# Optimization experiments

Hardware: AMD Instinct MI355X
Metric: run time of the kernel (lower is better)

Reference implementation:

```python
import jax, jax.numpy as jnp
import numpy as np

H = 16          # num_attention_heads
D = 1024        # input_size == hidden_size
HD = D // H     # attention_head_size = 64
EPS = 1e-12


def setup_inputs() -> dict:
    key = jax.random.key(0)
    ks = jax.random.split(key, 12)
    B, S = 4, 2048
    sc = 1.0 / np.sqrt(D)
    return {
        "x": jax.random.normal(ks[0], (B, S, D), jnp.float32),
        "y": jax.random.normal(ks[1], (B, S, D), jnp.float32),
        "Wq": jax.random.normal(ks[2], (D, D), jnp.float32) * sc,
        "bq": jnp.zeros((D,), jnp.float32),
        "Wk": jax.random.normal(ks[3], (D, D), jnp.float32) * sc,
        "bk": jnp.zeros((D,), jnp.float32),
        "Wv": jax.random.normal(ks[4], (D, D), jnp.float32) * sc,
        "bv": jnp.zeros((D,), jnp.float32),
        "Wd": jax.random.normal(ks[5], (D, D), jnp.float32) * sc,
        "bd": jnp.zeros((D,), jnp.float32),
        "gamma": jnp.ones((D,), jnp.float32),
        "beta": jnp.zeros((D,), jnp.float32),
        "debug": 0,
    }


def _split_heads(t):
    B, S, _ = t.shape
    return t.reshape(B, S, H, HD).transpose(0, 2, 1, 3)  # [B,H,S,hd]


def reference(x, y, Wq, bq, Wk, bk, Wv, bv, Wd, bd, gamma, beta, debug):
    # torch Linear: t @ W.T + b
    q = _split_heads(x @ Wq.T + bq)   # query from x
    k = _split_heads(y @ Wk.T + bk)   # key from y
    v = _split_heads(x @ Wv.T + bv)   # value from x (as in source)
    scores = jnp.einsum("bhqd,bhkd->bhqk", q, k) / np.sqrt(HD)
    probs = jax.nn.softmax(scores, axis=-1)  # dropout: eval mode (identity)
    ctx = jnp.einsum("bhqk,bhkd->bhqd", probs, v)
    B, _, S, _ = ctx.shape
    ctx = ctx.transpose(0, 2, 1, 3).reshape(B, S, D)
    h = ctx @ Wd.T + bd               # out_dropout: eval mode (identity)
    h = h + x
    u = h.mean(-1, keepdims=True)
    s = jnp.square(h - u).mean(-1, keepdims=True)
    h = (h - u) / jnp.sqrt(s + EPS)
    return gamma * h + beta
```

## Files before the change

kernel.cpp:

```cpp
#include <hip/hip_runtime.h>
#include <hip/hip_bf16.h>
#include <stdint.h>


typedef unsigned short ushortT;
typedef __attribute__((ext_vector_type(8))) __bf16 bf16x8;
typedef __attribute__((ext_vector_type(4))) float f32x4;
typedef __attribute__((ext_vector_type(16))) float f32x16;
typedef __attribute__((ext_vector_type(8))) unsigned short ushort8;
typedef __attribute__((ext_vector_type(4))) unsigned short ushort4v;

__device__ __forceinline__ unsigned short f2bf(float f) {
  union { float f; unsigned u; } x; x.f = f;
  unsigned r = (x.u + 0x7FFFu + ((x.u >> 16) & 1u)) >> 16;
  return (unsigned short)r;
}

__device__ __forceinline__ unsigned cvtpk_bf16(float lo, float hi) {
  unsigned r;
  asm("v_cvt_pk_bf16_f32 %0, %1, %2" : "=v"(r) : "v"(lo), "v"(hi));
  return r;
}

__device__ __forceinline__ void load_lds16(const void* g, void* l) {
  __builtin_amdgcn_global_load_lds(
      (const __attribute__((address_space(1))) void*)g,
      (__attribute__((address_space(3))) void*)l, 16, 0, 0);
}

__device__ __forceinline__ f32x4 mfma16(bf16x8 a, bf16x8 b, f32x4 c) {
  return __builtin_amdgcn_mfma_f32_16x16x32_bf16(a, b, c, 0, 0, 0);
}
__device__ __forceinline__ f32x16 mfma32(bf16x8 a, bf16x8 b, f32x16 c) {
  return __builtin_amdgcn_mfma_f32_32x32x16_bf16(a, b, c, 0, 0, 0);
}

__global__ __launch_bounds__(256) void k_cvt_all(
    const float* __restrict__ x, const float* __restrict__ y,
    const float* __restrict__ w0, const float* __restrict__ w1,
    const float* __restrict__ w2, const float* __restrict__ w3,
    ushortT* __restrict__ ox, ushortT* __restrict__ oy,
    ushortT* __restrict__ o0, ushortT* __restrict__ o1,
    ushortT* __restrict__ o2, ushortT* __restrict__ o3) {
  int b = blockIdx.x;
  const float* in;
  ushortT* out;
  int blk;
  if (b < 4096) {
    in = x; out = ox; blk = b;
  } else if (b < 8192) {
    in = y; out = oy; blk = b - 4096;
  } else {
    int z = (b - 8192) >> 9;
    blk = (b - 8192) & 511;
    in = (z == 0) ? w0 : (z == 1) ? w1 : (z == 2) ? w2 : w3;
    out = (z == 0) ? o0 : (z == 1) ? o1 : (z == 2) ? o2 : o3;
  }
  int i = blk * 256 + threadIdx.x;
  const float4* p = (const float4*)in;
  float4 u = p[(size_t)i * 2];
  float4 v = p[(size_t)i * 2 + 1];
  ushort8 o;
  o[0] = f2bf(u.x); o[1] = f2bf(u.y); o[2] = f2bf(u.z); o[3] = f2bf(u.w);
  o[4] = f2bf(v.x); o[5] = f2bf(v.y); o[6] = f2bf(v.z); o[7] = f2bf(v.w);
  *(ushort8*)(out + (size_t)i * 8) = o;
}

__global__ __launch_bounds__(256, 2) void k_gemm(
    const ushortT* __restrict__ xbf, const ushortT* __restrict__ ybf,
    const ushortT* __restrict__ wq, const ushortT* __restrict__ wk,
    const ushortT* __restrict__ wv, const ushortT* __restrict__ wd,
    const float* __restrict__ bq, const float* __restrict__ bk,
    const float* __restrict__ bv, const float* __restrict__ bd,
    const ushortT* __restrict__ ctx, const float* __restrict__ xres,
    ushortT* __restrict__ Qo, ushortT* __restrict__ Ko,
    ushortT* __restrict__ Vt, float* __restrict__ Ho, int mode_base) {
  __shared__ ushortT lA[2][128 * 64];
  __shared__ ushortT lB[2][128 * 64];
  const int t = threadIdx.x;
  const int lane = t & 63;
  const int w = t >> 6;
  const int wm = w >> 1, wn = w & 1;
  const int mode = mode_base + blockIdx.z;
  const int flat = blockIdx.x + (blockIdx.y << 3);
  const int xcd = flat & 7, j = flat >> 3;
  const int m0 = (xcd * 8 + (j >> 3)) * 128;
  const int n0 = (j & 7) * 128;

  const ushortT* A = (mode == 1) ? ybf : (mode == 3 ? ctx : xbf);
  const ushortT* W = (mode == 0) ? wq : (mode == 1 ? wk : (mode == 2 ? wv : wd));
  const float* bias = (mode == 0) ? bq : (mode == 1 ? bk : (mode == 2 ? bv : bd));

  f32x4 z = {0.f, 0.f, 0.f, 0.f};
  f32x4 acc[4][4];
#pragma unroll
  for (int i = 0; i < 4; ++i)
#pragma unroll
    for (int j2 = 0; j2 < 4; ++j2) acc[i][j2] = z;

  const int so = t * 16;
  const int srow = so >> 7;
  const int skb = (so & 127) ^ ((srow & 7) << 4);
  const ushortT* asrc = A + (size_t)(m0 + srow) * 1024 + (skb >> 1);
  const ushortT* wsrc = W + (size_t)(n0 + srow) * 1024 + (skb >> 1);

#define GSTAGE(buf, k0)                                                     \
  do {                                                                      \
    _Pragma("unroll")                                                       \
    for (int c = 0; c < 4; ++c) {                                           \
      load_lds16(asrc + (k0) + (size_t)c * 32 * 1024,                       \
                 (char*)&lA[buf][0] + c * 4096 + t * 16);                   \
      load_lds16(wsrc + (k0) + (size_t)c * 32 * 1024,                       \
                 (char*)&lB[buf][0] + c * 4096 + t * 16);                   \
    }                                                                       \
  } while (0)

  GSTAGE(0, 0);
  GSTAGE(1, 64);
  int cur = 0;
  for (int k0 = 0; k0 < 1024; k0 += 64) {
    if (k0 < 960) {
      asm volatile("s_waitcnt vmcnt(8)" ::: "memory");
    } else {
      asm volatile("s_waitcnt vmcnt(0)" ::: "memory");
    }
    __builtin_amdgcn_sched_barrier(0);
    __builtin_amdgcn_s_barrier();
    __builtin_amdgcn_sched_barrier(0);
#pragma unroll
    for (int kk = 0; kk < 2; ++kk) {
      bf16x8 af[4], bfr[4];
#pragma unroll
      for (int i = 0; i < 4; ++i) {
        int arow = wm * 64 + i * 16 + (lane & 15);
        int ak = ((kk * 32 + (lane >> 4) * 8) * 2) ^ ((arow & 7) << 4);
        af[i] = *(const bf16x8*)((const char*)&lA[cur][0] + arow * 128 + ak);
        int brow = wn * 64 + i * 16 + (lane & 15);
        int bk2 = ((kk * 32 + (lane >> 4) * 8) * 2) ^ ((brow & 7) << 4);
        bfr[i] = *(const bf16x8*)((const char*)&lB[cur][0] + brow * 128 + bk2);
      }
      __builtin_amdgcn_s_setprio(1);
#pragma unroll
      for (int i = 0; i < 4; ++i)
#pragma unroll
        for (int j2 = 0; j2 < 4; ++j2)
          acc[i][j2] = mfma16(af[i], bfr[j2], acc[i][j2]);
      __builtin_amdgcn_s_setprio(0);
    }
    __builtin_amdgcn_sched_barrier(0);
    __builtin_amdgcn_s_barrier();
    __builtin_amdgcn_sched_barrier(0);
    if (k0 + 128 < 1024) GSTAGE(cur, k0 + 128);
    cur ^= 1;
  }
#undef GSTAGE

  const int cm = wm * 64 + (lane >> 4) * 4;
  const int cn = wn * 64 + (lane & 15);
  if (mode == 3) {
#pragma unroll
    for (int mi = 0; mi < 4; ++mi)
#pragma unroll
      for (int ni = 0; ni < 4; ++ni) {
        int n = n0 + cn + ni * 16;
        float bn = bias[n];
#pragma unroll
        for (int r = 0; r < 4; ++r) {
          int m = m0 + cm + mi * 16 + r;
          Ho[(size_t)m * 1024 + n] =
              acc[mi][ni][r] + bn + xres[(size_t)m * 1024 + n];
        }
      }
  } else if (mode == 2) {
#pragma unroll
    for (int mi = 0; mi < 4; ++mi)
#pragma unroll
      for (int ni = 0; ni < 4; ++ni) {
        int n = n0 + cn + ni * 16;
        int hh = n >> 6, hd = n & 63;
        float bn = bias[n];
        int m_ = m0 + cm + mi * 16;
        int b = m_ >> 11, s = m_ & 2047;
        ushort4v pk;
#pragma unroll
        for (int r = 0; r < 4; ++r) pk[r] = f2bf(acc[mi][ni][r] + bn);
        *(ushort4v*)&Vt[(((size_t)(b * 16 + hh) * 64 + hd) << 11) + s] = pk;
      }
  } else {
    ushortT* O = (mode == 0) ? Qo : Ko;
    const float qs = (mode == 0) ? 0.18033688011112042f : 1.0f;
#pragma unroll
    for (int mi = 0; mi < 4; ++mi)
#pragma unroll
      for (int ni = 0; ni < 4; ++ni) {
        int n = n0 + cn + ni * 16;
        int hh = n >> 6, hd = n & 63;
        float bn = bias[n];
#pragma unroll
        for (int r = 0; r < 4; ++r) {
          int m = m0 + cm + mi * 16 + r;
          int b = m >> 11, s = m & 2047;
          O[(((size_t)(b * 16 + hh) * 2048 + s) << 6) + hd] =
              f2bf((acc[mi][ni][r] + bn) * qs);
        }
      }
  }
}

__global__ __launch_bounds__(256, 4) void k_attn(const ushortT* __restrict__ Q,
                                                 const ushortT* __restrict__ K,
                                                 const ushortT* __restrict__ Vt,
                                                 ushortT* __restrict__ ctx) {
  __shared__ ushortT lK[2][4096];
  __shared__ ushortT lV[2][4096];
  const int t = threadIdx.x, lane = t & 63, w = t >> 6;
  const int hi = lane >> 5, l31 = lane & 31;
  const int i0 = blockIdx.x;
  const int xcd = i0 & 7, j0 = i0 >> 3;
  const int bh = xcd * 8 + (j0 >> 4);
  const int qt = j0 & 15;
  const int q0 = qt * 128 + w * 32;

  const ushortT* Qb = Q + ((size_t)bh * 2048 + q0) * 64;
  const ushortT* Kb = K + (size_t)bh * 2048 * 64;
  const ushortT* Vb = Vt + (size_t)bh * 64 * 2048;

  bf16x8 qf[4];
#pragma unroll
  for (int dc = 0; dc < 4; ++dc)
    qf[dc] = *(const bf16x8*)(Qb + l31 * 64 + dc * 16 + hi * 8);

  union { unsigned short us[8]; bf16x8 v; } ones_u;
#pragma unroll
  for (int i = 0; i < 8; ++i) ones_u.us[i] = 0x3F80;

  f32x16 accO0, accO1, accL;
#pragma unroll
  for (int i = 0; i < 16; ++i) { accO0[i] = 0.f; accO1[i] = 0.f; accL[i] = 0.f; }

  const int srow = t >> 3;
  const int scolb = ((t & 7) * 16) ^ ((srow & 7) << 4);
  const ushortT* ksrc = Kb + srow * 64 + (scolb >> 1);
  const ushortT* vsrc = Vb + (size_t)srow * 2048 + (scolb >> 1);
  const int swz = (lane & 7) << 4;
  const int hs = (hi * 16) ^ swz;
  const int krowb = l31 * 128;

#define STAGE(buf, kk)                                                        \
  do {                                                                        \
    load_lds16(ksrc + (size_t)(kk) * 64, (char*)&lK[buf][0] + w * 1024);      \
    load_lds16(ksrc + 2048 + (size_t)(kk) * 64,                               \
               (char*)&lK[buf][0] + 4096 + w * 1024);                         \
    load_lds16(vsrc + (kk), (char*)&lV[buf][0] + w * 1024);                   \
    load_lds16(vsrc + 65536 + (kk), (char*)&lV[buf][0] + 4096 + w * 1024);    \
  } while (0)

  STAGE(0, 0);
  __syncthreads();
  int cur = 0;
  for (int k0 = 0; k0 < 2048; k0 += 64) {
    if (k0 + 64 < 2048) STAGE(cur ^ 1, k0 + 64);
    const char* lKc = (const char*)&lK[cur][0];
    const char* lVc = (const char*)&lV[cur][0];
#pragma unroll
    for (int kb = 0; kb < 2; ++kb) {
      f32x16 sc;
#pragma unroll
      for (int i = 0; i < 16; ++i) sc[i] = 0.f;
      __builtin_amdgcn_s_setprio(1);
#pragma unroll
      for (int dc = 0; dc < 4; ++dc) {
        bf16x8 kf = *(const bf16x8*)(lKc + kb * 4096 + krowb + ((dc * 32) ^ hs));
        sc = mfma32(kf, qf[dc], sc);
      }
      __builtin_amdgcn_s_setprio(0);
      float p[16];
#pragma unroll
      for (int r = 0; r < 16; ++r) p[r] = __builtin_amdgcn_exp2f(sc[r]);
      union { unsigned u[4]; bf16x8 v; } pa0, pa1;
#pragma unroll
      for (int i = 0; i < 4; ++i) {
        int base = (i >> 1) * 8 + (i & 1) * 2;
        unsigned a = cvtpk_bf16(p[base], p[base + 1]);
        unsigned b = cvtpk_bf16(p[base + 4], p[base + 5]);
        asm("v_permlane32_swap_b32 %0, %1" : "+v"(a), "+v"(b));
        if (i >> 1) { pa1.u[i & 1] = a; pa1.u[2 + (i & 1)] = b; }
        else        { pa0.u[i & 1] = a; pa0.u[2 + (i & 1)] = b; }
      }
      __builtin_amdgcn_s_setprio(1);
#pragma unroll
      for (int nb = 0; nb < 2; ++nb) {
        const char* vrow = lVc + (nb * 32 + l31) * 128;
        bf16x8 vf0 = *(const bf16x8*)(vrow + ((kb * 64) ^ hs));
        bf16x8 vf1 = *(const bf16x8*)(vrow + ((kb * 64 + 32) ^ hs));
        f32x16& ao = nb ? accO1 : accO0;
        ao = mfma32(pa0.v, vf0, ao);
        ao = mfma32(pa1.v, vf1, ao);
      }
      accL = mfma32(pa0.v, ones_u.v, accL);
      accL = mfma32(pa1.v, ones_u.v, accL);
      __builtin_amdgcn_s_setprio(0);
    }
    __syncthreads();
    cur ^= 1;
  }
#undef STAGE

  int b = bh >> 4, hh = bh & 15;
  ushortT* cb = ctx + ((size_t)(b * 2048 + q0)) * 1024 + hh * 64;
#pragma unroll
  for (int r = 0; r < 16; ++r) {
    int qm = (r & 3) + 8 * (r >> 2) + 4 * hi;
    float lr = 1.0f / accL[r];
    size_t rb = (size_t)qm * 1024;
    cb[rb + l31] = f2bf(accO0[r] * lr);
    cb[rb + 32 + l31] = f2bf(accO1[r] * lr);
  }
}

__global__ __launch_bounds__(256) void k_ln(const float* __restrict__ Hi,
                                            const float* __restrict__ gamma,
                                            const float* __restrict__ beta,
                                            float* __restrict__ out) {
  const int row = blockIdx.x, t = threadIdx.x, lane = t & 63, w = t >> 6;
  const float4* hp = (const float4*)(Hi + (size_t)row * 1024);
  float4 v = hp[t];
  float s1 = v.x + v.y + v.z + v.w;
  float s2 = v.x * v.x + v.y * v.y + v.z * v.z + v.w * v.w;
#pragma unroll
  for (int off = 1; off < 64; off <<= 1) {
    s1 += __shfl_xor(s1, off);
    s2 += __shfl_xor(s2, off);
  }
  __shared__ float red[8];
  if (lane == 0) { red[w] = s1; red[4 + w] = s2; }
  __syncthreads();
  s1 = red[0] + red[1] + red[2] + red[3];
  s2 = red[4] + red[5] + red[6] + red[7];
  float u = s1 * (1.f / 1024.f);
  float var = s2 * (1.f / 1024.f) - u * u;
  float rstd = rsqrtf(var + 1e-12f);
  float4 g = ((const float4*)gamma)[t];
  float4 bb = ((const float4*)beta)[t];
  float4 oo;
  oo.x = (v.x - u) * rstd * g.x + bb.x;
  oo.y = (v.y - u) * rstd * g.y + bb.y;
  oo.z = (v.z - u) * rstd * g.z + bb.z;
  oo.w = (v.w - u) * rstd * g.w + bb.w;
  ((float4*)(out + (size_t)row * 1024))[t] = oo;
}

extern "C" void kernel_launch(void* const* d_in, const int* in_sizes, int n_in,
                              void* d_out, int out_size, void* d_ws,
                              size_t ws_size, hipStream_t stream) {
  const float* x = (const float*)d_in[0];
  const float* y = (const float*)d_in[1];
  const float* Wq = (const float*)d_in[2];
  const float* bq = (const float*)d_in[3];
  const float* Wk = (const float*)d_in[4];
  const float* bk = (const float*)d_in[5];
  const float* Wv = (const float*)d_in[6];
  const float* bv = (const float*)d_in[7];
  const float* Wd = (const float*)d_in[8];
  const float* bd = (const float*)d_in[9];
  const float* gamma = (const float*)d_in[10];
  const float* beta = (const float*)d_in[11];

  char* ws = (char*)d_ws;
  ushortT* xbf = (ushortT*)(ws + 0);
  ushortT* ybf = (ushortT*)(ws + 16777216);
  ushortT* wqb = (ushortT*)(ws + 33554432);
  ushortT* wkb = (ushortT*)(ws + 35651584);
  ushortT* wvb = (ushortT*)(ws + 37748736);
  ushortT* wdb = (ushortT*)(ws + 39845888);
  ushortT* Qb = (ushortT*)(ws + 41943040);
  ushortT* Kb = (ushortT*)(ws + 58720256);
  ushortT* Vtb = (ushortT*)(ws + 75497472);
  ushortT* ctx = (ushortT*)(ws + 92274688);
  float* Hbuf = (float*)(ws + 0);

  k_cvt_all<<<10240, 256, 0, stream>>>(x, y, Wq, Wk, Wv, Wd, xbf, ybf, wqb,
                                       wkb, wvb, wdb);

  k_gemm<<<dim3(8, 64, 3), 256, 0, stream>>>(xbf, ybf, wqb, wkb, wvb, wdb, bq,
                                             bk, bv, bd, ctx, x, Qb, Kb, Vtb,
                                             Hbuf, 0);
  k_attn<<<1024, 256, 0, stream>>>(Qb, Kb, Vtb, ctx);
  k_gemm<<<dim3(8, 64, 1), 256, 0, stream>>>(xbf, ybf, wqb, wkb, wvb, wdb, bq,
                                             bk, bv, bd, ctx, x, Qb, Kb, Vtb,
                                             Hbuf, 3);
  k_ln<<<8192, 256, 0, stream>>>(Hbuf, gamma, beta, (float*)d_out);
}
```

Baseline: 200.8 us.

## Restructure GEMM to 256x128 tiles with 8 waves and finer-grained interleaved prefetch

The projection GEMM now uses 512-thread blocks computing 256x128 output tiles instead of 128x128. Each wave holds an 8x2 grid of MFMA accumulators, and the K loop is split into four sub-phases. Each sub-phase interleaves LDS fragment reads, partial global-to-LDS prefetch of the next stage, and MFMAs, separated by barriers. The goal is better operand reuse per block and overlap of memory traffic with compute. The cost is the loss of the previous XCD-aware block remapping, more barriers per iteration, and a different LDS swizzle that must stay correct.

Result: slower. 254.6 us (+26.8%).

```diff
diff --git a/kernel.cpp b/kernel.cpp
--- a/kernel.cpp
+++ b/kernel.cpp
@@ -66,7 +66,7 @@
   *(ushort8*)(out + (size_t)i * 8) = o;
 }
 
-__global__ __launch_bounds__(256, 2) void k_gemm(
+__global__ __launch_bounds__(512, 2) void k_gemm(
     const ushortT* __restrict__ xbf, const ushortT* __restrict__ ybf,
     const ushortT* __restrict__ wq, const ushortT* __restrict__ wk,
     const ushortT* __restrict__ wv, const ushortT* __restrict__ wd,
@@ -75,111 +75,161 @@
     const ushortT* __restrict__ ctx, const float* __restrict__ xres,
     ushortT* __restrict__ Qo, ushortT* __restrict__ Ko,
     ushortT* __restrict__ Vt, float* __restrict__ Ho, int mode_base) {
-  __shared__ ushortT lA[2][128 * 64];
-  __shared__ ushortT lB[2][128 * 64];
+  __shared__ char lA[2 * 32768];
+  __shared__ char lB[2 * 16384];
   const int t = threadIdx.x;
   const int lane = t & 63;
   const int w = t >> 6;
-  const int wm = w >> 1, wn = w & 1;
+  const int wm = w >> 2, wn = w & 3;
   const int mode = mode_base + blockIdx.z;
-  const int flat = blockIdx.x + (blockIdx.y << 3);
-  const int xcd = flat & 7, j = flat >> 3;
-  const int m0 = (xcd * 8 + (j >> 3)) * 128;
-  const int n0 = (j & 7) * 128;
+  const int bid = blockIdx.x;
+  const int m0 = (bid >> 3) * 256;
+  const int n0 = (bid & 7) * 128;
 
   const ushortT* A = (mode == 1) ? ybf : (mode == 3 ? ctx : xbf);
   const ushortT* W = (mode == 0) ? wq : (mode == 1 ? wk : (mode == 2 ? wv : wd));
   const float* bias = (mode == 0) ? bq : (mode == 1 ? bk : (mode == 2 ? bv : bd));
 
   f32x4 z = {0.f, 0.f, 0.f, 0.f};
-  f32x4 acc[4][4];
-#pragma unroll
-  for (int i = 0; i < 4; ++i)
-#pragma unroll
-    for (int j2 = 0; j2 < 4; ++j2) acc[i][j2] = z;
-
-  const int so = t * 16;
-  const int srow = so >> 7;
-  const int skb = (so & 127) ^ ((srow & 7) << 4);
-  const ushortT* asrc = A + (size_t)(m0 + srow) * 1024 + (skb >> 1);
-  const ushortT* wsrc = W + (size_t)(n0 + srow) * 1024 + (skb >> 1);
-
-#define GSTAGE(buf, k0)                                                     \
-  do {                                                                      \
-    _Pragma("unroll")                                                       \
-    for (int c = 0; c < 4; ++c) {                                           \
-      load_lds16(asrc + (k0) + (size_t)c * 32 * 1024,                       \
-                 (char*)&lA[buf][0] + c * 4096 + t * 16);                   \
-      load_lds16(wsrc + (k0) + (size_t)c * 32 * 1024,                       \
-                 (char*)&lB[buf][0] + c * 4096 + t * 16);                   \
-    }                                                                       \
-  } while (0)
-
-  GSTAGE(0, 0);
-  GSTAGE(1, 64);
-  int cur = 0;
-  for (int k0 = 0; k0 < 1024; k0 += 64) {
-    if (k0 < 960) {
-      asm volatile("s_waitcnt vmcnt(8)" ::: "memory");
-    } else {
+  f32x4 acc[8][2];
+#pragma unroll
+  for (int i = 0; i < 8; ++i) {
+    acc[i][0] = z;
+    acc[i][1] = z;
+  }
+
+  const int ar_s = t >> 2;
+  const int aq = t & 3;
+  const int tb = t * 16;
+  const ushortT* abase =
+      A + (size_t)(m0 + ar_s) * 1024 + ((aq ^ (ar_s & 3)) * 8);
+  const ushortT* bbase =
+      W + (size_t)(n0 + ar_s) * 1024 + ((aq ^ (ar_s & 3)) * 8);
+
+#define STG_A(buf, tt, h, c)                                          \
+  load_lds16(abase + (size_t)(c) * 131072 + (tt) * 64 + (h) * 32,     \
+             lA + (buf) * 32768 + (h) * 16384 + (c) * 8192 + tb)
+#define STG_B(buf, tt, h)                                             \
+  load_lds16(bbase + (tt) * 64 + (h) * 32,                            \
+             lB + (buf) * 16384 + (h) * 8192 + tb)
+
+  const int aswz = ((lane >> 4) ^ (lane & 3)) << 4;
+  const int arb = (wm * 128 + (lane & 15)) * 64 + aswz;
+  const int brb = (wn * 32 + (lane & 15)) * 64 + aswz;
+
+  STG_A(0, 0, 0, 0); STG_A(0, 0, 0, 1); STG_B(0, 0, 0);
+  STG_A(0, 0, 1, 0); STG_A(0, 0, 1, 1); STG_B(0, 0, 1);
+  asm volatile("s_waitcnt vmcnt(3)" ::: "memory");
+  __builtin_amdgcn_s_barrier();
+  __builtin_amdgcn_sched_barrier(0);
+
+  for (int tt = 0; tt < 16; ++tt) {
+    const int cur = tt & 1, nxt = cur ^ 1;
+    const bool pf = (tt < 15);
+    const char* lAc = lA + cur * 32768;
+    const char* lBc = lB + cur * 16384;
+    bf16x8 b0[2], b1[2], af[4];
+
+#pragma unroll
+    for (int ni = 0; ni < 2; ++ni)
+      b0[ni] = *(const bf16x8*)(lBc + brb + ni * 1024);
+#pragma unroll
+    for (int mi = 0; mi < 4; ++mi)
+      af[mi] = *(const bf16x8*)(lAc + arb + mi * 1024);
+    if (pf) { STG_A(nxt, tt + 1, 0, 0); STG_A(nxt, tt + 1, 0, 1); }
+    __builtin_amdgcn_s_barrier();
+    __builtin_amdgcn_s_setprio(1);
+#pragma unroll
+    for (int mi = 0; mi < 4; ++mi) {
+      acc[mi][0] = mfma16(af[mi], b0[0], acc[mi][0]);
+      acc[mi][1] = mfma16(af[mi], b0[1], acc[mi][1]);
+    }
+    __builtin_amdgcn_s_setprio(0);
+    __builtin_amdgcn_s_barrier();
+
+#pragma unroll
+    for (int mi = 0; mi < 4; ++mi)
+      af[mi] = *(const bf16x8*)(lAc + arb + (4 + mi) * 1024);
+    if (pf) STG_B(nxt, tt + 1, 0);
+    __builtin_amdgcn_s_barrier();
+    __builtin_amdgcn_s_setprio(1);
+#pragma unroll
+    for (int mi = 0; mi < 4; ++mi) {
+      acc[4 + mi][0] = mfma16(af[mi], b0[0], acc[4 + mi][0]);
+      acc[4 + mi][1] = mfma16(af[mi], b0[1], acc[4 + mi][1]);
+    }
+    __builtin_amdgcn_s_setprio(0);
+    if (pf)
+      asm volatile("s_waitcnt vmcnt(3)" ::: "memory");
+    else
       asm volatile("s_waitcnt vmcnt(0)" ::: "memory");
+    __builtin_amdgcn_s_barrier();
+    __builtin_amdgcn_sched_barrier(0);
+
+#pragma unroll
+    for (int ni = 0; ni < 2; ++ni)
+      b1[ni] = *(const bf16x8*)(lBc + 8192 + brb + ni * 1024);
+#pragma unroll
+    for (int mi = 0; mi < 4; ++mi)
+      af[mi] = *(const bf16x8*)(lAc + 16384 + arb + mi * 1024);
+    if (pf) { STG_A(nxt, tt + 1, 1, 0); STG_A(nxt, tt + 1, 1, 1); }
+    __builtin_amdgcn_s_barrier();
+    __builtin_amdgcn_s_setprio(1);
+#pragma unroll
+    for (int mi = 0; mi < 4; ++mi) {
+      acc[mi][0] = mfma16(af[mi], b1[0], acc[mi][0]);
+      acc[mi][1] = mfma16(af[mi], b1[1], acc[mi][1]);
     }
+    __builtin_amdgcn_s_setprio(0);
+    __builtin_amdgcn_s_barrier();
+
+#pragma unroll
+    for (int mi = 0; mi < 4; ++mi)
+      af[mi] = *(const bf16x8*)(lAc + 16384 + arb + (4 + mi) * 1024);
+    if (pf) STG_B(nxt, tt + 1, 1);
+    __builtin_amdgcn_s_barrier();
+    __builtin_amdgcn_s_setprio(1);
+#pragma unroll
+    for (int mi = 0; mi < 4; ++mi) {
+      acc[4 + mi][0] = mfma16(af[mi], b1[0], acc[4 + mi][0]);
+      acc[4 + mi][1] = mfma16(af[mi], b1[1], acc[4 + mi][1]);
+    }
+    __builtin_amdgcn_s_setprio(0);
+    if (pf)
+      asm volatile("s_waitcnt vmcnt(3)" ::: "memory");
+    else
+      asm volatile("s_waitcnt vmcnt(0)" ::: "memory");
+    __builtin_amdgcn_s_barrier();
     __builtin_amdgcn_sched_barrier(0);
-    __builtin_amdgcn_s_barrier();
-    __builtin_amdgcn_sched_barrier(0);
-#pragma unroll
-    for (int kk = 0; kk < 2; ++kk) {
-      bf16x8 af[4], bfr[4];
-#pragma unroll
-      for (int i = 0; i < 4; ++i) {
-        int arow = wm * 64 + i * 16 + (lane & 15);
-        int ak = ((kk * 32 + (lane >> 4) * 8) * 2) ^ ((arow & 7) << 4);
-        af[i] = *(const bf16x8*)((const char*)&lA[cur][0] + arow * 128 + ak);
-        int brow = wn * 64 + i * 16 + (lane & 15);
-        int bk2 = ((kk * 32 + (lane >> 4) * 8) * 2) ^ ((brow & 7) << 4);
-        bfr[i] = *(const bf16x8*)((const char*)&lB[cur][0] + brow * 128 + bk2);
-      }
-      __builtin_amdgcn_s_setprio(1);
-#pragma unroll
-      for (int i = 0; i < 4; ++i)
-#pragma unroll
-        for (int j2 = 0; j2 < 4; ++j2)
-          acc[i][j2] = mfma16(af[i], bfr[j2], acc[i][j2]);
-      __builtin_amdgcn_s_setprio(0);
-    }
-    __builtin_amdgcn_sched_barrier(0);
-    __builtin_amdgcn_s_barrier();
-    __builtin_amdgcn_sched_barrier(0);
-    if (k0 + 128 < 1024) GSTAGE(cur, k0 + 128);
-    cur ^= 1;
-  }
-#undef GSTAGE
-
-  const int cm = wm * 64 + (lane >> 4) * 4;
-  const int cn = wn * 64 + (lane & 15);
+  }
+#undef STG_A
+#undef STG_B
+
+  const int cmb = wm * 128 + (lane >> 4) * 4;
+  const int cnb = wn * 32 + (lane & 15);
   if (mode == 3) {
 #pragma unroll
-    for (int mi = 0; mi < 4; ++mi)
-#pragma unroll
-      for (int ni = 0; ni < 4; ++ni) {
-        int n = n0 + cn + ni * 16;
+    for (int mi = 0; mi < 8; ++mi)
+#pragma unroll
+      for (int ni = 0; ni < 2; ++ni) {
+        int n = n0 + cnb + ni * 16;
         float bn = bias[n];
 #pragma unroll
         for (int r = 0; r < 4; ++r) {
-          int m = m0 + cm + mi * 16 + r;
+          int m = m0 + cmb + mi * 16 + r;
           Ho[(size_t)m * 1024 + n] =
               acc[mi][ni][r] + bn + xres[(size_t)m * 1024 + n];
         }
       }
   } else if (mode == 2) {
 #pragma unroll
-    for (int mi = 0; mi < 4; ++mi)
-#pragma unroll
-      for (int ni = 0; ni < 4; ++ni) {
-        int n = n0 + cn + ni * 16;
+    for (int mi = 0; mi < 8; ++mi)
+#pragma unroll
+      for (int ni = 0; ni < 2; ++ni) {
+        int n = n0 + cnb + ni * 16;
         int hh = n >> 6, hd = n & 63;
         float bn = bias[n];
-        int m_ = m0 + cm + mi * 16;
+        int m_ = m0 + cmb + mi * 16;
         int b = m_ >> 11, s = m_ & 2047;
         ushort4v pk;
 #pragma unroll
@@ -190,15 +240,15 @@
     ushortT* O = (mode == 0) ? Qo : Ko;
     const float qs = (mode == 0) ? 0.18033688011112042f : 1.0f;
 #pragma unroll
-    for (int mi = 0; mi < 4; ++mi)
-#pragma unroll
-      for (int ni = 0; ni < 4; ++ni) {
-        int n = n0 + cn + ni * 16;
+    for (int mi = 0; mi < 8; ++mi)
+#pragma unroll
+      for (int ni = 0; ni < 2; ++ni) {
+        int n = n0 + cnb + ni * 16;
         int hh = n >> 6, hd = n & 63;
         float bn = bias[n];
 #pragma unroll
         for (int r = 0; r < 4; ++r) {
-          int m = m0 + cm + mi * 16 + r;
+          int m = m0 + cmb + mi * 16 + r;
           int b = m >> 11, s = m & 2047;
           O[(((size_t)(b * 16 + hh) * 2048 + s) << 6) + hd] =
               f2bf((acc[mi][ni][r] + bn) * qs);
@@ -382,12 +432,12 @@
   k_cvt_all<<<10240, 256, 0, stream>>>(x, y, Wq, Wk, Wv, Wd, xbf, ybf, wqb,
                                        wkb, wvb, wdb);
 
-  k_gemm<<<dim3(8, 64, 3), 256, 0, stream>>>(xbf, ybf, wqb, wkb, wvb, wdb, bq,
-                                             bk, bv, bd, ctx, x, Qb, Kb, Vtb,
-                                             Hbuf, 0);
+  k_gemm<<<dim3(256, 1, 3), 512, 0, stream>>>(xbf, ybf, wqb, wkb, wvb, wdb,
+                                              bq, bk, bv, bd, ctx, x, Qb, Kb,
+                                              Vtb, Hbuf, 0);
   k_attn<<<1024, 256, 0, stream>>>(Qb, Kb, Vtb, ctx);
-  k_gemm<<<dim3(8, 64, 1), 256, 0, stream>>>(xbf, ybf, wqb, wkb, wvb, wdb, bq,
-                                             bk, bv, bd, ctx, x, Qb, Kb, Vtb,
-                                             Hbuf, 3);
+  k_gemm<<<dim3(256, 1, 1), 512, 0, stream>>>(xbf, ybf, wqb, wkb, wvb, wdb,
+                                              bq, bk, bv, bd, ctx, x, Qb, Kb,
+                                              Vtb, Hbuf, 3);
   k_ln<<<8192, 256, 0, stream>>>(Hbuf, gamma, beta, (float*)d_out);
 }
```
